# Kernel tuning notes

Measured on AMD Instinct MI355X. Metric: run time of the kernel, lower is better.

Reference implementation:

```python
import jax, jax.numpy as jnp
import numpy as np
import math

HID, H = 384, 4
D = HID // H  # 96, HGT head dim
N_T = [2048, 2048, 2048, 1024, 1024]  # user_turn, ai_turn, stance, pressure, belief
OFF = [0, 2048, 4096, 6144, 7168]
NTOT = 8192
# (src_type, dst_type, num_edges)
EDGES = [(0, 1, 32768), (1, 0, 32768), (1, 2, 32768), (2, 2, 32768),
         (0, 3, 16384), (3, 1, 32768), (1, 4, 16384), (4, 2, 32768)]
E_OFF = np.concatenate([[0], np.cumsum([c for _, _, c in EDGES])]).tolist()


def _gelu(x):
    return jax.nn.gelu(x, approximate=False)


def _ln(x, g, b, eps=1e-5):
    m = x.mean(-1, keepdims=True)
    v = ((x - m) ** 2).mean(-1, keepdims=True)
    return (x - m) * jax.lax.rsqrt(v + eps) * g + b


def _mha(q_in, kv_in, Wqkv, bqkv, Wo, bo):
    # torch nn.MultiheadAttention (batch_first, batch=1); Wqkv stored [E, 3E]
    E = HID
    q = (q_in @ Wqkv[:, :E] + bqkv[:E]).reshape(-1, H, D)
    k = (kv_in @ Wqkv[:, E:2 * E] + bqkv[E:2 * E]).reshape(-1, H, D)
    v = (kv_in @ Wqkv[:, 2 * E:] + bqkv[2 * E:]).reshape(-1, H, D)
    s = jnp.einsum('qhd,khd->hqk', q, k) / math.sqrt(D)
    w = jax.nn.softmax(s, axis=-1)
    o = jnp.einsum('hqk,khd->qhd', w, v).reshape(-1, E)
    return o @ Wo + bo


def _forward(x_user, x_ai, x_stance, x_pressure, x_belief,
             hgt_Wkqv, hgt_bkqv, hgt_Wout, hgt_bout, hgt_krel, hgt_vrel, hgt_prel, hgt_skip,
             ln_g, ln_b, sp_W, sp_b, sp_lng, sp_lnb, fc0_W, fc0_b, bn_g, bn_b,
             tq_W, tq_b, tk_W, tk_b, tv_W, tv_b, mha_Wqkv, mha_bqkv, mha_Wo, mha_bo,
             c1_W, c1_b, c2_W, c2_b, op_W, op_b, as1_W, as1_b, as2_W, as2_b,
             sc1_W, sc1_b, sc2_W, sc2_b, cl1_W, cl1_b, cl_lng, cl_lnb,
             cl2_W, cl2_b, cl3_W, cl3_b, tp_W, tp_b, edge_src, edge_dst):
    xs = [x_user, x_ai, x_stance, x_pressure, x_belief]
    for l in range(2):
        kqv = [x @ hgt_Wkqv[l, t] + hgt_bkqv[l, t] for t, x in enumerate(xs)]
        kk = [a[:, :HID].reshape(-1, H, D) for a in kqv]
        qq = [a[:, HID:2 * HID].reshape(-1, H, D) for a in kqv]
        vv = [a[:, 2 * HID:].reshape(-1, H, D) for a in kqv]
        al, msg, dgl = [], [], []
        for r, (s, d, cnt) in enumerate(EDGES):
            si = edge_src[E_OFF[r]:E_OFF[r + 1]]
            di = edge_dst[E_OFF[r]:E_OFF[r + 1]]
            ke = jnp.einsum('ehd,hdf->ehf', kk[s][si], hgt_krel[l, r])
            ve = jnp.einsum('ehd,hdf->ehf', vv[s][si], hgt_vrel[l, r])
            a = (qq[d][di] * ke).sum(-1) * hgt_prel[l, r] / math.sqrt(D)  # [E_r, H]
            al.append(a); msg.append(ve); dgl.append(di + OFF[d])
        a = jnp.concatenate(al); ve = jnp.concatenate(msg); dg = jnp.concatenate(dgl)
        mx = jax.ops.segment_max(a, dg, num_segments=NTOT)
        ex = jnp.exp(a - mx[dg])
        den = jax.ops.segment_sum(ex, dg, num_segments=NTOT)
        w = ex / den[dg]
        agg = jax.ops.segment_sum(ve * w[:, :, None], dg, num_segments=NTOT).reshape(NTOT, HID)
        new = []
        for t, x in enumerate(xs):
            o = _gelu(agg[OFF[t]:OFF[t] + N_T[t]]) @ hgt_Wout[l, t] + hgt_bout[l, t]
            g = jax.nn.sigmoid(hgt_skip[l, t])
            new.append(g * o + (1 - g) * x)
        xs = [_ln(_gelu(v), ln_g[t], ln_b[t]) for t, v in enumerate(new)]
    user_h, ai_h, stance_h, pressure_h, belief_h = xs

    # ---- StanceTrajectoryEncoder ----
    hs = _gelu(_ln(stance_h @ sp_W + sp_b, sp_lng, sp_lnb))

    def bn(x, i):  # eval-mode BatchNorm1d, running stats (0, 1)
        return x * (bn_g[i] / math.sqrt(1.0 + 1e-5)) + bn_b[i]

    xg = jax.nn.relu(bn(hs @ fc0_W + fc0_b, 0))
    Ns = hs.shape[0]
    for i in range(2):  # SGFormer TransConv layers (linear global attention)
        q = (xg @ tq_W[i] + tq_b[i]).reshape(Ns, H, HID)
        k = (xg @ tk_W[i] + tk_b[i]).reshape(Ns, H, HID)
        v = (xg @ tv_W[i] + tv_b[i]).reshape(Ns, H, HID)
        qn = q / jnp.linalg.norm(q)  # global Frobenius norm, as in SGFormer
        kn = k / jnp.linalg.norm(k)
        kvs = jnp.einsum('lhm,lhd->hmd', kn, v)
        num = jnp.einsum('nhm,hmd->nhd', qn, kvs) + Ns * v
        dnm = jnp.einsum('nhm,hm->nh', qn, kn.sum(0))[:, :, None] + Ns
        z = (num / dnm).mean(axis=1)  # mean over heads
        xg = jax.nn.relu(bn(0.5 * z + 0.5 * xg, i + 1))  # residual alpha=0.5
    h_mixed = 0.7 * hs + 0.3 * xg
    traj = _mha(h_mixed, h_mixed, mha_Wqkv[1], mha_bqkv[1], mha_Wo[1], mha_bo[1])
    traj_summary = traj.mean(0, keepdims=True)  # [1, HID]
    ci = h_mixed.T[None]  # [1, C, L]
    dn = ('NCH', 'OIH', 'NCH')
    c = jax.lax.conv_general_dilated(ci, c1_W, (1,), [(1, 1)], dimension_numbers=dn) + c1_b[None, :, None]
    c = _gelu(c)
    c = jax.lax.conv_general_dilated(c, c2_W, (1,), [(1, 1)], dimension_numbers=dn) + c2_b[None, :, None]
    c = _gelu(c)
    decay_summary = c.mean(axis=2)  # [1, HID//2]
    traj_emb = jnp.concatenate([traj_summary, decay_summary], -1) @ op_W + op_b

    # ---- PressureResponseModule ----
    ai_ctx = _mha(ai_h, user_h, mha_Wqkv[0], mha_bqkv[0], mha_Wo[0], mha_bo[0])
    ml = min(N_T[1], N_T[0])
    comb = jnp.concatenate([ai_h[:ml], user_h[:ml]], -1)
    pscores = jax.nn.sigmoid((jax.nn.relu(comb @ as1_W + as1_b) @ as2_W + as2_b)[:, 0])
    ai_pooled = ai_ctx.mean(0, keepdims=True)

    # ---- belief attention + stance comparison + classifier ----
    bctx = _mha(ai_h, belief_h, mha_Wqkv[2], mha_bqkv[2], mha_Wo[2], mha_bo[2]).mean(0, keepdims=True)
    sd_in = jnp.concatenate([stance_h[0:1], stance_h[-1:]], -1)
    stance_delta = jax.nn.relu(sd_in @ sc1_W + sc1_b) @ sc2_W + sc2_b
    comb2 = jnp.concatenate([traj_emb, ai_pooled, bctx, stance_delta], -1)  # [1, 1344]
    z = jax.nn.relu(_ln(comb2 @ cl1_W + cl1_b, cl_lng, cl_lnb))
    z = jax.nn.relu(z @ cl2_W + cl2_b)
    logits = (z @ cl3_W + cl3_b).reshape(())
    decay = jax.nn.sigmoid(logits)
    per_turn = jax.nn.sigmoid((ai_ctx @ tp_W + tp_b)[:, 0])
    return logits, decay, per_turn, pscores


def setup_inputs() -> dict:
    key = jax.random.key(0)
    ks = iter(jax.random.split(key, 128))

    def P(shape, fan_in):
        return jax.random.normal(next(ks), shape, jnp.float32) / np.float32(math.sqrt(fan_in))

    inp = {}
    for name, n in zip(['x_user', 'x_ai', 'x_stance', 'x_pressure', 'x_belief'], N_T):
        inp[name] = jax.random.normal(next(ks), (n, HID), jnp.float32)
    inp['hgt_Wkqv'] = P((2, 5, HID, 3 * HID), HID)
    inp['hgt_bkqv'] = jnp.zeros((2, 5, 3 * HID))
    inp['hgt_Wout'] = P((2, 5, HID, HID), HID)
    inp['hgt_bout'] = jnp.zeros((2, 5, HID))
    inp['hgt_krel'] = P((2, 8, H, D, D), D)
    inp['hgt_vrel'] = P((2, 8, H, D, D), D)
    inp['hgt_prel'] = jnp.ones((2, 8, H))
    inp['hgt_skip'] = jnp.ones((2, 5))
    inp['ln_g'] = jnp.ones((5, HID)); inp['ln_b'] = jnp.zeros((5, HID))
    inp['sp_W'] = P((HID, HID), HID); inp['sp_b'] = jnp.zeros((HID,))
    inp['sp_lng'] = jnp.ones((HID,)); inp['sp_lnb'] = jnp.zeros((HID,))
    inp['fc0_W'] = P((HID, HID), HID); inp['fc0_b'] = jnp.zeros((HID,))
    inp['bn_g'] = jnp.ones((3, HID)); inp['bn_b'] = jnp.zeros((3, HID))
    for nm in ['tq', 'tk', 'tv']:
        inp[nm + '_W'] = P((2, HID, H * HID), HID)
        inp[nm + '_b'] = jnp.zeros((2, H * HID))
    inp['mha_Wqkv'] = P((3, HID, 3 * HID), HID)
    inp['mha_bqkv'] = jnp.zeros((3, 3 * HID))
    inp['mha_Wo'] = P((3, HID, HID), HID)
    inp['mha_bo'] = jnp.zeros((3, HID))
    inp['c1_W'] = P((HID, HID, 3), HID * 3); inp['c1_b'] = jnp.zeros((HID,))
    inp['c2_W'] = P((HID // 2, HID, 3), HID * 3); inp['c2_b'] = jnp.zeros((HID // 2,))
    inp['op_W'] = P((HID + HID // 2, HID), HID + HID // 2); inp['op_b'] = jnp.zeros((HID,))
    inp['as1_W'] = P((2 * HID, HID), 2 * HID); inp['as1_b'] = jnp.zeros((HID,))
    inp['as2_W'] = P((HID, 1), HID); inp['as2_b'] = jnp.zeros((1,))
    inp['sc1_W'] = P((2 * HID, HID), 2 * HID); inp['sc1_b'] = jnp.zeros((HID,))
    inp['sc2_W'] = P((HID, HID // 2), HID); inp['sc2_b'] = jnp.zeros((HID // 2,))
    CIN = 3 * HID + HID // 2
    inp['cl1_W'] = P((CIN, HID), CIN); inp['cl1_b'] = jnp.zeros((HID,))
    inp['cl_lng'] = jnp.ones((HID,)); inp['cl_lnb'] = jnp.zeros((HID,))
    inp['cl2_W'] = P((HID, HID // 2), HID); inp['cl2_b'] = jnp.zeros((HID // 2,))
    inp['cl3_W'] = P((HID // 2, 1), HID // 2); inp['cl3_b'] = jnp.zeros((1,))
    inp['tp_W'] = P((HID, 1), HID); inp['tp_b'] = jnp.zeros((1,))
    srcs, dsts = [], []
    for (s, d, cnt) in EDGES:
        srcs.append(jax.random.randint(next(ks), (cnt,), 0, N_T[s], jnp.int32))
        dsts.append(jax.random.randint(next(ks), (cnt,), 0, N_T[d], jnp.int32))
    inp['edge_src'] = jnp.concatenate(srcs)
    inp['edge_dst'] = jnp.concatenate(dsts)
    return inp


def reference(x_user, x_ai, x_stance, x_pressure, x_belief,
              hgt_Wkqv, hgt_bkqv, hgt_Wout, hgt_bout, hgt_krel, hgt_vrel, hgt_prel, hgt_skip,
              ln_g, ln_b, sp_W, sp_b, sp_lng, sp_lnb, fc0_W, fc0_b, bn_g, bn_b,
              tq_W, tq_b, tk_W, tk_b, tv_W, tv_b, mha_Wqkv, mha_bqkv, mha_Wo, mha_bo,
              c1_W, c1_b, c2_W, c2_b, op_W, op_b, as1_W, as1_b, as2_W, as2_b,
              sc1_W, sc1_b, sc2_W, sc2_b, cl1_W, cl1_b, cl_lng, cl_lnb,
              cl2_W, cl2_b, cl3_W, cl3_b, tp_W, tp_b, edge_src, edge_dst):
    return _forward(x_user, x_ai, x_stance, x_pressure, x_belief,
                    hgt_Wkqv, hgt_bkqv, hgt_Wout, hgt_bout, hgt_krel, hgt_vrel, hgt_prel, hgt_skip,
                    ln_g, ln_b, sp_W, sp_b, sp_lng, sp_lnb, fc0_W, fc0_b, bn_g, bn_b,
                    tq_W, tq_b, tk_W, tk_b, tv_W, tv_b, mha_Wqkv, mha_bqkv, mha_Wo, mha_bo,
                    c1_W, c1_b, c2_W, c2_b, op_W, op_b, as1_W, as1_b, as2_W, as2_b,
                    sc1_W, sc1_b, sc2_W, sc2_b, cl1_W, cl1_b, cl_lng, cl_lnb,
                    cl2_W, cl2_b, cl3_W, cl3_b, tp_W, tp_b, edge_src, edge_dst)
```

## Files before the change

kernel.cpp:

```cpp
#include <hip/hip_runtime.h>
#include <hip/hip_bf16.h>

#define NEDGE 229376
#define NTOT  8192
#define BNCONST 0.9999950000374997f
#define ISQ96   0.10206207261596575f

__constant__ int c_NT[5]     = {2048,2048,2048,1024,1024};
__constant__ int c_OFFS[5]   = {0,2048,4096,6144,7168};
__constant__ int c_ESRC[8]   = {0,1,1,2,0,3,1,4};
__constant__ int c_EDST[8]   = {1,0,2,2,3,1,4,2};
__constant__ int c_EOFF[9]   = {0,32768,65536,98304,131072,147456,180224,196608,229376};
__constant__ int c_RELROW[8] = {0,2048,4096,6144,8192,10240,11264,13312};

static const int h_NT[5]   = {2048,2048,2048,1024,1024};
static const int h_OFFS[5] = {0,2048,4096,6144,7168};

__device__ inline float gelu_f(float x){ return 0.5f*x*(1.0f+erff(x*0.70710678118654752f)); }
__device__ inline float sigm(float x){ return 1.0f/(1.0f+expf(-x)); }
__device__ inline float wsum64(float v){
  #pragma unroll
  for (int s=32;s>0;s>>=1) v += __shfl_xor(v, s, 64);
  return v;
}
// ... 18 lines not shown
__device__ inline float rgsum(float v){
  v += __shfl_xor(v, 1, 64);
  v += __shfl_xor(v, 2, 64);
  v += __shfl_xor(v, 4, 64);
  v += __shfl_xor(v, 8, 64);
  return v;
}


__global__ void k_mix(const float* __restrict__ a, const float* __restrict__ b,
                      float* __restrict__ c, int n, float fa, float fb){
  int i = blockIdx.x*256 + threadIdx.x;
  if (i < n) c[i] = fa*a[i] + fb*b[i];
}

__global__ void k_comb(const float* __restrict__ ai, const float* __restrict__ user,
                       float* __restrict__ cb){
  int i = blockIdx.x*256 + threadIdx.x;
  if (i >= 2048*768) return;
  int n = i / 768, c = i - n*768;
  cb[i] = (c < 384) ? ai[n*384 + c] : user[n*384 + (c-384)];
}


__global__ void k_edge_pre(const int* __restrict__ esrc, const int* __restrict__ edst,
                           int* edg, int* esr, int* erl, int* cnt){
  int e = blockIdx.x*256 + threadIdx.x;
  if (e >= NEDGE) return;
  int r = 0;
  #pragma unroll
  for (int q=1;q<8;q++) if (e >= c_EOFF[q]) r = q;
  int dg = c_OFFS[c_EDST[r]] + edst[e];
  edg[e] = dg;
  esr[e] = c_RELROW[r] + esrc[e];
  erl[e] = r;
  atomicAdd(&cnt[dg], 1);
}

__global__ __launch_bounds__(1024) void k_scan(const int* __restrict__ cnt, int* __restrict__ off){
  __shared__ int sh[1024];
  int tid = threadIdx.x;
  int base = tid*8;
  int loc[8]; int run = 0;
  #pragma unroll
  for (int i=0;i<8;i++){ loc[i] = run; run += cnt[base+i]; }
  sh[tid] = run;
  __syncthreads();
  for (int d=1; d<1024; d<<=1){
    int v = (tid >= d) ? sh[tid-d] : 0;
    __syncthreads();
    sh[tid] += v;
    __syncthreads();
  }
  int pre = (tid==0) ? 0 : sh[tid-1];
  #pragma unroll
  for (int i=0;i<8;i++) off[base+i] = pre + loc[i];
  if (tid==1023) off[8192] = sh[1023];
}

__global__ void k_scatter(const int* __restrict__ edg, const int* __restrict__ off,
                          int* cnt2, int* csr){
  int e = blockIdx.x*256 + threadIdx.x;
  if (e >= NEDGE) return;
  int dg = edg[e];
  int pos = off[dg] + atomicAdd(&cnt2[dg], 1);
  csr[pos] = e;
}


__global__ __launch_bounds__(256) void gemm_f(
    const float* __restrict__ A, int lda, const float* __restrict__ B, int ldb,
    const float* __restrict__ bias, const float* __restrict__ cs, const float* __restrict__ csh,
    float kmul, float* __restrict__ C, int ldc, int M, int N, int K, int act, int agelu)
{
  __shared__ float As[2][16][68];
  __shared__ float Bs[2][16][68];
  int tid = threadIdx.x;
  int tx = tid & 15, ty = tid >> 4;
  int am = tid >> 2, ak = (tid & 3) * 4;
  int bk = tid >> 4, bn = (tid & 15) * 4;
  int m0 = blockIdx.y * 64, n0 = blockIdx.x * 64;
  int gmA = m0 + am;
  int gnB = n0 + bn;
  int ntiles = K >> 4;
  float4 ra, rb;
  float acc[4][4] = {};

  auto fetch = [&](int kk){
    if (gmA < M){
      ra = *reinterpret_cast<const float4*>(&A[(size_t)gmA*lda + kk + ak]);
      if (agelu){ ra.x=gelu_f(ra.x); ra.y=gelu_f(ra.y); ra.z=gelu_f(ra.z); ra.w=gelu_f(ra.w); }
    } else ra = make_float4(0.f,0.f,0.f,0.f);
    if (gnB + 3 < N){
      rb = *reinterpret_cast<const float4*>(&B[(size_t)(kk + bk)*ldb + gnB]);
    } else {
      rb.x = (gnB   < N) ? B[(size_t)(kk + bk)*ldb + gnB  ] : 0.f;
      rb.y = (gnB+1 < N) ? B[(size_t)(kk + bk)*ldb + gnB+1] : 0.f;
      rb.z = (gnB+2 < N) ? B[(size_t)(kk + bk)*ldb + gnB+2] : 0.f;
      rb.w = (gnB+3 < N) ? B[(size_t)(kk + bk)*ldb + gnB+3] : 0.f;
    }
  };
  auto stage = [&](int b){
    As[b][ak  ][am] = ra.x;
    As[b][ak+1][am] = ra.y;
    As[b][ak+2][am] = ra.z;
    As[b][ak+3][am] = ra.w;
    *reinterpret_cast<float4*>(&Bs[b][bk][bn]) = rb;
  };

  fetch(0);
  stage(0);
  __syncthreads();
  for (int t = 0; t < ntiles; t++){
    int cur = t & 1;
    if (t + 1 < ntiles) fetch((t+1) << 4);
    #pragma unroll
    for (int k = 0; k < 16; k++) {
      float4 a4 = *reinterpret_cast<const float4*>(&As[cur][k][ty*4]);
      float4 b4 = *reinterpret_cast<const float4*>(&Bs[cur][k][tx*4]);
      float a[4] = {a4.x, a4.y, a4.z, a4.w};
      float b[4] = {b4.x, b4.y, b4.z, b4.w};
      #pragma unroll
      for (int i=0;i<4;i++)
        #pragma unroll
        for (int j=0;j<4;j++) acc[i][j] += a[i]*b[j];
    }
    if (t + 1 < ntiles) stage(cur ^ 1);
    __syncthreads();
  }
  #pragma unroll
  for (int i=0;i<4;i++){
    int gm = m0 + ty*4 + i; if (gm >= M) continue;
    #pragma unroll
    for (int j=0;j<4;j++){
      int gn = n0 + tx*4 + j; if (gn >= N) continue;
      float v = acc[i][j];
      if (bias) v += bias[gn];
      float s = kmul;
      if (cs) s *= cs[gn];
      v *= s;
      if (csh) v += csh[gn];
      if (act==1) v = fmaxf(v, 0.f);
      else if (act==2) v = gelu_f(v);
      C[(size_t)gm*ldc + gn] = v;
    }
  }
}

__global__ __launch_bounds__(256) void gemm128(
    const float* __restrict__ A, int lda, int sAz,
    const float* __restrict__ B, int ldb, int sBz,
    const float* __restrict__ bias, int sbz,
    float* __restrict__ C, int ldc, int sCz,
    int M, int N, int K, int act, int agelu, int tsel)
{
  __shared__ float As[2][16][132];
  __shared__ float Bs[2][16][132];
  int tid = threadIdx.x;
  int tx = tid & 15, ty = tid >> 4;
  int am = tid >> 1, ak = (tid & 1) * 8;
  int bk = tid >> 4, bn = (tid & 15) * 8;
  int m0 = blockIdx.y * 128, n0 = blockIdx.x * 128;
  int z = blockIdx.z;
  const float* Ab = A + (size_t)z * sAz;
  const float* Bb = B + (size_t)z * sBz;
  const float* bb = bias ? (bias + (size_t)z * sbz) : nullptr;
  float* Cb = C + (size_t)z * sCz;
  if (tsel){
    int t = row_type(m0);
    Bb = B + (size_t)t * sBz;
    bb = bias ? (bias + (size_t)t * sbz) : nullptr;
  }
  int gmA = m0 + am, gnB = n0 + bn;
  int ntiles = K >> 4;
  float4 ra0, ra1, rb0, rb1;
  float acc[8][8] = {};

  auto fetch = [&](int kk){
    if (gmA < M){
      ra0 = *reinterpret_cast<const float4*>(&Ab[(size_t)gmA*lda + kk + ak]);
      ra1 = *reinterpret_cast<const float4*>(&Ab[(size_t)gmA*lda + kk + ak + 4]);
      if (agelu){
        ra0.x=gelu_f(ra0.x); ra0.y=gelu_f(ra0.y); ra0.z=gelu_f(ra0.z); ra0.w=gelu_f(ra0.w);
        ra1.x=gelu_f(ra1.x); ra1.y=gelu_f(ra1.y); ra1.z=gelu_f(ra1.z); ra1.w=gelu_f(ra1.w);
      }
    } else {
      ra0 = make_float4(0.f,0.f,0.f,0.f); ra1 = ra0;
    }
    if (gnB + 7 < N){
      rb0 = *reinterpret_cast<const float4*>(&Bb[(size_t)(kk + bk)*ldb + gnB]);
      rb1 = *reinterpret_cast<const float4*>(&Bb[(size_t)(kk + bk)*ldb + gnB + 4]);
    } else {
      const float* bp = &Bb[(size_t)(kk + bk)*ldb];
      rb0.x = (gnB   < N) ? bp[gnB  ] : 0.f;
      rb0.y = (gnB+1 < N) ? bp[gnB+1] : 0.f;
      rb0.z = (gnB+2 < N) ? bp[gnB+2] : 0.f;
      rb0.w = (gnB+3 < N) ? bp[gnB+3] : 0.f;
      rb1.x = (gnB+4 < N) ? bp[gnB+4] : 0.f;
      rb1.y = (gnB+5 < N) ? bp[gnB+5] : 0.f;
      rb1.z = (gnB+6 < N) ? bp[gnB+6] : 0.f;
      rb1.w = (gnB+7 < N) ? bp[gnB+7] : 0.f;
    }
  };
  auto stage = [&](int b){
    As[b][ak  ][am] = ra0.x;
    As[b][ak+1][am] = ra0.y;
    As[b][ak+2][am] = ra0.z;
    As[b][ak+3][am] = ra0.w;
    As[b][ak+4][am] = ra1.x;
    As[b][ak+5][am] = ra1.y;
    As[b][ak+6][am] = ra1.z;
    As[b][ak+7][am] = ra1.w;
    *reinterpret_cast<float4*>(&Bs[b][bk][bn  ]) = rb0;
    *reinterpret_cast<float4*>(&Bs[b][bk][bn+4]) = rb1;
  };

  fetch(0);
  stage(0);
  __syncthreads();
  for (int t = 0; t < ntiles; t++){
    int cur = t & 1;
    if (t + 1 < ntiles) fetch((t+1) << 4);
    #pragma unroll
    for (int k = 0; k < 16; k++) {
      float4 a0 = *reinterpret_cast<const float4*>(&As[cur][k][ty*8]);
      float4 a1 = *reinterpret_cast<const float4*>(&As[cur][k][ty*8+4]);
      float4 b0 = *reinterpret_cast<const float4*>(&Bs[cur][k][tx*8]);
      float4 b1 = *reinterpret_cast<const float4*>(&Bs[cur][k][tx*8+4]);
      float a[8] = {a0.x,a0.y,a0.z,a0.w,a1.x,a1.y,a1.z,a1.w};
      float b[8] = {b0.x,b0.y,b0.z,b0.w,b1.x,b1.y,b1.z,b1.w};
      #pragma unroll
      for (int i=0;i<8;i++)
        #pragma unroll
        for (int j=0;j<8;j++) acc[i][j] += a[i]*b[j];
    }
    if (t + 1 < ntiles) stage(cur ^ 1);
    __syncthreads();
  }

  bool fullN = (n0 + 127 < N);
  #pragma unroll
  for (int i=0;i<8;i++){
    int gm = m0 + ty*8 + i; if (gm >= M) continue;
    float v[8];
    #pragma unroll
    for (int j=0;j<8;j++){
      float x = acc[i][j];
      if (bb){
        int gn = n0 + tx*8 + j;
        if (gn < N) x += bb[gn];
      }
      if (act==1) x = fmaxf(x, 0.f);
      else if (act==2) x = gelu_f(x);
      v[j] = x;
    }
    if (fullN){
      *reinterpret_cast<float4*>(&Cb[(size_t)gm*ldc + n0 + tx*8    ]) = make_float4(v[0],v[1],v[2],v[3]);
      *reinterpret_cast<float4*>(&Cb[(size_t)gm*ldc + n0 + tx*8 + 4]) = make_float4(v[4],v[5],v[6],v[7]);
    } else {
      #pragma unroll
      for (int j=0;j<8;j++){
        int gn = n0 + tx*8 + j; if (gn >= N) continue;
        Cb[(size_t)gm*ldc + gn] = v[j];
      }
    }
  }
}

__global__ __launch_bounds__(256) void gemm_rel(
    const float* __restrict__ KQV_, const float* __restrict__ krel_l,
    const float* __restrict__ vrel_l, float* __restrict__ KE_, float* __restrict__ VE_)
{
  int z = blockIdx.z;
  int w = z & 1, h = (z >> 1) & 3, r = z >> 3;
  int s = c_ESRC[r];
  int Ns = c_NT[s];
  int m0 = blockIdx.y * 64;
  if (m0 >= Ns) return;
  int n0 = blockIdx.x * 64;
  const float* A = KQV_ + (size_t)c_OFFS[s]*1152 + (w ? 768 : 0) + h*96;
  const float* B = (w ? vrel_l : krel_l) + (size_t)(r*4 + h)*9216;
  float* C = (w ? VE_ : KE_) + (size_t)c_RELROW[r]*384 + h*96;

  __shared__ float As[2][16][68];
  __shared__ float Bs[2][16][68];
  int tid = threadIdx.x;
  int tx = tid & 15, ty = tid >> 4;
  int am = tid >> 2, ak = (tid & 3) * 4;
  int bk = tid >> 4, bn = (tid & 15) * 4;
  int gmA = m0 + am;
  int gnB = n0 + bn;
  float4 ra, rb;
  float acc[4][4] = {};

  auto fetch = [&](int kk){
    ra = (gmA < Ns) ? *reinterpret_cast<const float4*>(&A[(size_t)gmA*1152 + kk + ak])
                    : make_float4(0.f,0.f,0.f,0.f);
    if (gnB + 3 < 96){
      rb = *reinterpret_cast<const float4*>(&B[(size_t)(kk + bk)*96 + gnB]);
    } else {
      rb.x = (gnB   < 96) ? B[(size_t)(kk + bk)*96 + gnB  ] : 0.f;
      rb.y = (gnB+1 < 96) ? B[(size_t)(kk + bk)*96 + gnB+1] : 0.f;
      rb.z = (gnB+2 < 96) ? B[(size_t)(kk + bk)*96 + gnB+2] : 0.f;
      rb.w = (gnB+3 < 96) ? B[(size_t)(kk + bk)*96 + gnB+3] : 0.f;
    }
  };
  auto stage = [&](int b){
    As[b][ak  ][am] = ra.x;
    As[b][ak+1][am] = ra.y;
    As[b][ak+2][am] = ra.z;
    As[b][ak+3][am] = ra.w;
    *reinterpret_cast<float4*>(&Bs[b][bk][bn]) = rb;
  };

  fetch(0);
  stage(0);
  __syncthreads();
  for (int t = 0; t < 6; t++){
    int cur = t & 1;
    if (t + 1 < 6) fetch((t+1) << 4);
    #pragma unroll
    for (int k = 0; k < 16; k++) {
      float4 a4 = *reinterpret_cast<const float4*>(&As[cur][k][ty*4]);
      float4 b4 = *reinterpret_cast<const float4*>(&Bs[cur][k][tx*4]);
      float a[4] = {a4.x, a4.y, a4.z, a4.w};
      float b[4] = {b4.x, b4.y, b4.z, b4.w};
      #pragma unroll
      for (int i=0;i<4;i++)
        #pragma unroll
        for (int j=0;j<4;j++) acc[i][j] += a[i]*b[j];
    }
    if (t + 1 < 6) stage(cur ^ 1);
    __syncthreads();
  }
  #pragma unroll
  for (int i=0;i<4;i++){
    int gm = m0 + ty*4 + i; if (gm >= Ns) continue;
    #pragma unroll
    for (int j=0;j<4;j++){
      int gn = n0 + tx*4 + j; if (gn >= 96) continue;
      C[(size_t)gm*384 + gn] = acc[i][j];
    }
  }
}

__global__ __launch_bounds__(256) void gemm_atb_ks(
    const float* __restrict__ A0, int lda, const float* __restrict__ B0, int ldb,
    float* __restrict__ C0, int ldc, int M, int N, int L,
    int hsA, int hsB, int hsC, int nch)
{
  __shared__ float As[2][16][68];
  __shared__ float Bs[2][16][68];
  int h = blockIdx.z / nch, c = blockIdx.z % nch;
  const float* A = A0 + (size_t)h*hsA;
  const float* B = B0 + (size_t)h*hsB;
  float* C = C0 + (size_t)h*hsC;
  int l0 = c*256;
  int tid = threadIdx.x;
  int tx = tid & 15, ty = tid >> 4;
  int sl = tid >> 4, sq = (tid & 15) * 4;
  int m0 = blockIdx.y * 64, n0 = blockIdx.x * 64;
  int gmA = m0 + sq, gnB = n0 + sq;
  int ntiles = 16;
  float4 ra, rb;
  float acc[4][4] = {};

  auto fetch = [&](int ll){
    if (gmA + 3 < M){
      ra = *reinterpret_cast<const float4*>(&A[(size_t)(ll + sl)*lda + gmA]);
    } else {
      ra.x = (gmA   < M) ? A[(size_t)(ll + sl)*lda + gmA  ] : 0.f;
      ra.y = (gmA+1 < M) ? A[(size_t)(ll + sl)*lda + gmA+1] : 0.f;
      ra.z = (gmA+2 < M) ? A[(size_t)(ll + sl)*lda + gmA+2] : 0.f;
      ra.w = (gmA+3 < M) ? A[(size_t)(ll + sl)*lda + gmA+3] : 0.f;
    }
    if (gnB + 3 < N){
      rb = *reinterpret_cast<const float4*>(&B[(size_t)(ll + sl)*ldb + gnB]);
    } else {
      rb.x = (gnB   < N) ? B[(size_t)(ll + sl)*ldb + gnB  ] : 0.f;
      rb.y = (gnB+1 < N) ? B[(size_t)(ll + sl)*ldb + gnB+1] : 0.f;
      rb.z = (gnB+2 < N) ? B[(size_t)(ll + sl)*ldb + gnB+2] : 0.f;
      rb.w = (gnB+3 < N) ? B[(size_t)(ll + sl)*ldb + gnB+3] : 0.f;
    }
  };
  auto stage = [&](int b){
    *reinterpret_cast<float4*>(&As[b][sl][sq]) = ra;
    *reinterpret_cast<float4*>(&Bs[b][sl][sq]) = rb;
  };

  fetch(l0);
  stage(0);
  __syncthreads();
  for (int t = 0; t < ntiles; t++){
    int cur = t & 1;
    if (t + 1 < ntiles) fetch(l0 + ((t+1) << 4));
    #pragma unroll
    for (int l = 0; l < 16; l++) {
      float4 a4 = *reinterpret_cast<const float4*>(&As[cur][l][ty*4]);
      float4 b4 = *reinterpret_cast<const float4*>(&Bs[cur][l][tx*4]);
      float a[4] = {a4.x, a4.y, a4.z, a4.w};
      float b[4] = {b4.x, b4.y, b4.z, b4.w};
      #pragma unroll
      for (int i=0;i<4;i++)
        #pragma unroll
        for (int j=0;j<4;j++) acc[i][j] += a[i]*b[j];
    }
    if (t + 1 < ntiles) stage(cur ^ 1);
    __syncthreads();
  }
  #pragma unroll
  for (int i=0;i<4;i++){
    int gm = m0 + ty*4 + i; if (gm >= M) continue;
    #pragma unroll
    for (int j=0;j<4;j++){
      int gn = n0 + tx*4 + j; if (gn >= N) continue;
      atomicAdd(&C[(size_t)gm*ldc + gn], acc[i][j]);
// ... 373 lines not shown
    const float* __restrict__ w, const float* __restrict__ b, float* __restrict__ out, int M){
  int r = blockIdx.x*4 + (threadIdx.x>>6);
  if (r >= M) return;
  int lane = threadIdx.x & 63;
  const float* a = A + (size_t)r*lda;
  float p = 0.f;
  for (int k = lane; k < K; k += 64) p += a[k]*w[k];
  p = wsum64(p);
  if (lane==0) out[r] = sigm(p + b[0]);
}

__global__ __launch_bounds__(64) void k_final(const float* __restrict__ z2,
    const float* __restrict__ w, const float* __restrict__ b, float* __restrict__ out){
  int lane = threadIdx.x;
  float p = 0.f;
  for (int k = lane; k < 192; k += 64) p += z2[k]*w[k];
  p = wsum64(p);
  if (lane==0){
    float l = p + b[0];
    out[0] = l;
    out[1] = sigm(l);
  }
}


extern "C" void kernel_launch(void* const* d_in, const int* in_sizes, int n_in,
                              void* d_out, int out_size, void* d_ws, size_t ws_size,
                              hipStream_t stream)
{
  const float* xin[5] = {(const float*)d_in[0], (const float*)d_in[1], (const float*)d_in[2],
                         (const float*)d_in[3], (const float*)d_in[4]};
  const float* Wkqv=(const float*)d_in[5];  const float* bkqv=(const float*)d_in[6];
  const float* Wout=(const float*)d_in[7];  const float* bout=(const float*)d_in[8];
  const float* krel=(const float*)d_in[9];  const float* vrel=(const float*)d_in[10];
  const float* prel=(const float*)d_in[11]; const float* skp =(const float*)d_in[12];
  const float* lng =(const float*)d_in[13]; const float* lnb =(const float*)d_in[14];
  const float* sp_W=(const float*)d_in[15]; const float* sp_b=(const float*)d_in[16];
  const float* sp_lng=(const float*)d_in[17]; const float* sp_lnb=(const float*)d_in[18];
  const float* fc0_W=(const float*)d_in[19]; const float* fc0_b=(const float*)d_in[20];
  const float* bn_g=(const float*)d_in[21]; const float* bn_b=(const float*)d_in[22];
  const float* tq_W=(const float*)d_in[23]; const float* tq_b=(const float*)d_in[24];
  const float* tk_W=(const float*)d_in[25]; const float* tk_b=(const float*)d_in[26];
  const float* tv_W=(const float*)d_in[27]; const float* tv_b=(const float*)d_in[28];
  const float* mWqkv=(const float*)d_in[29]; const float* mbqkv=(const float*)d_in[30];
  const float* mWo=(const float*)d_in[31];  const float* mbo=(const float*)d_in[32];
  const float* c1W=(const float*)d_in[33];  const float* c1b=(const float*)d_in[34];
  const float* c2W=(const float*)d_in[35];  const float* c2b=(const float*)d_in[36];
  const float* opW=(const float*)d_in[37];  const float* opb=(const float*)d_in[38];
  const float* as1W=(const float*)d_in[39]; const float* as1b=(const float*)d_in[40];
  const float* as2W=(const float*)d_in[41]; const float* as2b=(const float*)d_in[42];
  const float* sc1W=(const float*)d_in[43]; const float* sc1b=(const float*)d_in[44];
  const float* sc2W=(const float*)d_in[45]; const float* sc2b=(const float*)d_in[46];
  const float* cl1W=(const float*)d_in[47]; const float* cl1b=(const float*)d_in[48];
  const float* cllng=(const float*)d_in[49]; const float* cllnb=(const float*)d_in[50];
  const float* cl2W=(const float*)d_in[51]; const float* cl2b=(const float*)d_in[52];
  const float* cl3W=(const float*)d_in[53]; const float* cl3b=(const float*)d_in[54];
  const float* tpW=(const float*)d_in[55];  const float* tpb=(const float*)d_in[56];
  const int* e_src=(const int*)d_in[57];  const int* e_dst=(const int*)d_in[58];
  float* out = (float*)d_out;

  char* ws = (char*)d_ws;
  size_t off_b = 0;
  auto alloc = [&](size_t bytes)->char*{
    char* r = ws + off_b;
    off_b = (off_b + bytes + 255) & ~(size_t)255;
    return r;
  };
  float* X    = (float*)alloc((size_t)8192*384*4);
  float* KQV  = (float*)alloc((size_t)8192*1152*4);
  float* KE   = (float*)alloc((size_t)14336*384*4);
  float* VE   = (float*)alloc((size_t)14336*384*4);
  float* AGG  = (float*)alloc((size_t)8192*384*4);
  float* EA   = (float*)alloc((size_t)NEDGE*4*4);
  int* edg    = (int*)alloc((size_t)NEDGE*4);
  int* esr    = (int*)alloc((size_t)NEDGE*4);
  int* erl    = (int*)alloc((size_t)NEDGE*4);
  int* csr    = (int*)alloc((size_t)NEDGE*4);
  int* cnt    = (int*)alloc(8192*4);
  int* cnt2   = (int*)alloc(8192*4);
  int* coff   = (int*)alloc(8193*4);
  unsigned* EMX = (unsigned*)alloc(8192*4*4);
  float* EDEN = (float*)alloc(8192*4*4);
  float* SM   = (float*)alloc(65536);
  float* GT   = (float*)alloc(20*384*4);
  if (off_b > ws_size) return;

  float* SQSK = SM;
  float* TRAJSUM = SM + 8;
  float* DECAYSUM = SM + 392;
  float* TEMB = SM + 600;
  float* AIPOOL = SM + 984;
  float* BCTXV = SM + 1368;
  float* SDELT = SM + 1752;
  float* SDIN = SM + 2048;
  float* T1   = SM + 2816;
  float* Z1   = SM + 3200;
  float* Zb   = SM + 3584;
  float* Z2   = SM + 3968;
  float* KSUM = SM + 4224;
  float* DNM  = SM + 6144;

  float* QB = KQV;
  float* KB = KQV + (size_t)2048*1536;
  float* VB = KQV + (size_t)2*2048*1536;
  float* MQKV = KQV;
  float* AO = KQV + (size_t)2*2048*1536;
  float* ZNUM = KE;
  float* OWT = KE;
  float* OPART = KE;
  float* MLBUF = KE + (size_t)3200000;
  float* IMC = KE;
  float* WT  = KE + (size_t)2400000;
  float* HS = VE;
  float* XG = VE + (size_t)2048*384;
  float* HM = VE + (size_t)2*2048*384;
  float* C1O = VE + (size_t)3*2048*384;
  float* TRAJ = VE + (size_t)4*2048*384;
  float* AICTX = VE + (size_t)5*2048*384;
  float* C2O = VE + (size_t)6*2048*384;
  float* TMPA = AGG;
  float* CB = AGG;
  float* PT = AGG + (size_t)2048*768;
  float* KVS = AGG + (size_t)2048*1152;

  dim3 B256(256);
  auto gemm = [&](const float* A, int lda, const float* Bw, int ldb, const float* bias,
                  const float* cs, const float* csh, float kmul,
                  float* C, int ldc, int M, int N, int K, int act, int agelu){
    dim3 g((N+63)/64, (M+63)/64);
    gemm_f<<<g, B256, 0, stream>>>(A, lda, Bw, ldb, bias, cs, csh, kmul, C, ldc, M, N, K, act, agelu);
  };
  auto gemv = [&](const float* in, int K, const float* W, int ldw, const float* b,
                  float* o, int N, int act){
    int nk = (K + 79) / 80; if (nk > 20) nk = 20; if (nk < 1) nk = 1;
    k_gemv_ks<<<dim3((N+63)/64, nk), B256, 0, stream>>>(in, K, W, ldw, GT, N);
    k_gemv_fin<<<dim3((N+255)/256), B256, 0, stream>>>(GT, nk, b, o, N, act);
  };

  hipMemsetAsync(cnt, 0, 8192*4, stream);
  hipMemsetAsync(cnt2, 0, 8192*4, stream);
  k_edge_pre<<<dim3(NEDGE/256), B256, 0, stream>>>(e_src, e_dst, edg, esr, erl, cnt);
  k_scan<<<dim3(1), dim3(1024), 0, stream>>>(cnt, coff);
  k_scatter<<<dim3(NEDGE/256), B256, 0, stream>>>(edg, coff, cnt2, csr);

  for (int t=0;t<5;t++)
    hipMemcpyAsync(X + (size_t)h_OFFS[t]*384, xin[t], (size_t)h_NT[t]*384*4,
                   hipMemcpyDeviceToDevice, stream);

  for (int l=0;l<2;l++){
    gemm128<<<dim3(9, 64), B256, 0, stream>>>(
        X, 384, 0,
        Wkqv + (size_t)l*5*442368, 1152, 442368,
        bkqv + (size_t)l*5*1152, 1152,
        KQV, 1152, 0, 8192, 1152, 384, 0, 0, 1 );
    gemm_rel<<<dim3(2,32,64), B256, 0, stream>>>(
        KQV, krel + (size_t)l*294912, vrel + (size_t)l*294912, KE, VE);
    k_escore<<<dim3(NEDGE/4), B256, 0, stream>>>(KQV, KE, edg, esr, erl, prel + (size_t)l*32, EA);
    hipMemsetAsync(EMX, 0, 8192*4*4, stream);
    hipMemsetAsync(EDEN, 0, 8192*4*4, stream);
    k_segmax<<<dim3(NEDGE*4/256), B256, 0, stream>>>(EA, edg, EMX);
    k_expsum<<<dim3(NEDGE*4/256), B256, 0, stream>>>(EA, edg, EMX, EDEN);
    k_agg<<<dim3(NTOT), dim3(128), 0, stream>>>(EA, VE, EDEN, csr, coff, esr, AGG);
    gemm128<<<dim3(3, 64), B256, 0, stream>>>(
        AGG, 384, 0,
        Wout + (size_t)l*5*147456, 384, 147456,
        bout + (size_t)l*5*384, 384,
        OWT, 384, 0, 8192, 384, 384, 0, 1 , 1 );
    k_gateln<<<dim3(NTOT), dim3(128), 0, stream>>>(OWT, X, skp + l*5, lng, lnb);
  }

  const float* user_h   = X;
  const float* ai_h     = X + (size_t)2048*384;
  const float* stance_h = X + (size_t)4096*384;
  const float* belief_h = X + (size_t)7168*384;

  gemm(stance_h, 384, sp_W, 384, sp_b, nullptr, nullptr, 1.f, TMPA, 384, 2048, 384, 384, 0, 0);
  k_lnrow<<<dim3(2048), dim3(128), 0, stream>>>(TMPA, HS, sp_lng, sp_lnb, 0 );
  gemm(HS, 384, fc0_W, 384, fc0_b, bn_g, bn_b, BNCONST, XG, 384, 2048, 384, 384, 1 , 0);

  for (int i=0;i<2;i++){
    gemm128<<<dim3(12,16), B256, 0, stream>>>(
        XG, 384, 0, tq_W + (size_t)i*589824, 1536, 0,
        tq_b + (size_t)i*1536, 0, QB, 1536, 0, 2048, 1536, 384, 0, 0, 0);
    gemm128<<<dim3(12,16), B256, 0, stream>>>(
        XG, 384, 0, tk_W + (size_t)i*589824, 1536, 0,
        tk_b + (size_t)i*1536, 0, KB, 1536, 0, 2048, 1536, 384, 0, 0, 0);
    gemm128<<<dim3(12,16), B256, 0, stream>>>(
        XG, 384, 0, tv_W + (size_t)i*589824, 1536, 0,
        tv_b + (size_t)i*1536, 0, VB, 1536, 0, 2048, 1536, 384, 0, 0, 0);
    hipMemsetAsync(SQSK, 0, 8, stream);
    k_sumsq<<<dim3(512), B256, 0, stream>>>(QB, 2048*1536, SQSK);
    k_sumsq<<<dim3(512), B256, 0, stream>>>(KB, 2048*1536, SQSK+1);
    hipMemsetAsync(KSUM, 0, 1536*4, stream);
    k_colsum<<<dim3(6,8), B256, 0, stream>>>(KB, 2048, 1536, 1.0f, KSUM);
    k_dnm<<<dim3(2048), B256, 0, stream>>>(QB, KSUM, SQSK, DNM);
    hipMemsetAsync(KVS, 0, (size_t)4*147456*4, stream);
    gemm_atb_ks<<<dim3(6,6,32), B256, 0, stream>>>(KB, 1536, VB, 1536, KVS, 384,
        384, 384, 2048, 384, 384, 147456, 8);
    gemm128<<<dim3(3,16,4), B256, 0, stream>>>(
        QB, 1536, 384, KVS, 384, 147456,
        nullptr, 0, ZNUM, 1536, 384, 2048, 384, 384, 0, 0, 0);
    k_zcomb<<<dim3(3072), B256, 0, stream>>>(ZNUM, VB, DNM, SQSK, XG,
        bn_g + (size_t)(i+1)*384, bn_b + (size_t)(i+1)*384);
  }

  k_mix<<<dim3(3072), B256, 0, stream>>>(HS, XG, HM, 2048*384, 0.7f, 0.3f);

  auto run_mha = [&](const float* qin, int nq, const float* kvin, int nkv, int mi, float* OUT){
    const float* Wq = mWqkv + (size_t)mi*442368;
    const float* bq = mbqkv + (size_t)mi*1152;
    gemm(qin, 384, Wq, 1152, bq, nullptr, nullptr, 1.f, MQKV, 1152, nq, 384, 384, 0, 0);
    gemm(kvin, 384, Wq + 384, 1152, bq + 384, nullptr, nullptr, 1.f, MQKV + 384, 1152, nkv, 768, 384, 0, 0);
    int nch = nkv / 512;
    fa_kernel<<<dim3(nq/64, 4, nch), B256, 0, stream>>>(MQKV, nq, OPART, MLBUF);
    k_famerge<<<dim3((4*nq*96 + 255)/256), B256, 0, stream>>>(OPART, MLBUF, AO, nq, nch);
    gemm(AO, 384, mWo + (size_t)mi*147456, 384, mbo + (size_t)mi*384,
         nullptr, nullptr, 1.f, OUT, 384, nq, 384, 384, 0, 0);
  };

  run_mha(HM, 2048, HM, 2048, 1, TRAJ);
  hipMemsetAsync(TRAJSUM, 0, 576*4, stream);
  k_colsum<<<dim3(2,8), B256, 0, stream>>>(TRAJ, 2048, 384, 1.0f/2048.0f, TRAJSUM);

  k_im2col<<<dim3(2048*1152/256), B256, 0, stream>>>(HM, IMC);
  k_wtr<<<dim3((384*1152+255)/256), B256, 0, stream>>>(c1W, WT, 384);
  gemm(IMC, 1152, WT, 384, c1b, nullptr, nullptr, 1.f, C1O, 384, 2048, 384, 1152, 2 , 0);
  k_im2col<<<dim3(2048*1152/256), B256, 0, stream>>>(C1O, IMC);
  k_wtr<<<dim3((192*1152+255)/256), B256, 0, stream>>>(c2W, WT, 192);
  gemm(IMC, 1152, WT, 192, c2b, nullptr, nullptr, 1.f, C2O, 192, 2048, 192, 1152, 2 , 0);
  k_colsum<<<dim3(1,8), B256, 0, stream>>>(C2O, 2048, 192, 1.0f/2048.0f, DECAYSUM);

  gemv(TRAJSUM, 576, opW, 384, opb, TEMB, 384, 0);

  run_mha(ai_h, 2048, user_h, 2048, 0, AICTX);
  hipMemsetAsync(AIPOOL, 0, 384*4, stream);
  k_colsum<<<dim3(2,8), B256, 0, stream>>>(AICTX, 2048, 384, 1.0f/2048.0f, AIPOOL);

  k_comb<<<dim3(6144), B256, 0, stream>>>(ai_h, user_h, CB);
  gemm(CB, 768, as1W, 384, as1b, nullptr, nullptr, 1.f, PT, 384, 2048, 384, 768, 1, 0);
  k_rowdot<<<dim3(512), B256, 0, stream>>>(PT, 384, 384, as2W, as2b, out + 2 + 2048, 2048);

  run_mha(ai_h, 2048, belief_h, 1024, 2, TRAJ);
  hipMemsetAsync(BCTXV, 0, 384*4, stream);
  k_colsum<<<dim3(2,8), B256, 0, stream>>>(TRAJ, 2048, 384, 1.0f/2048.0f, BCTXV);

  hipMemcpyAsync(SDIN, stance_h, 384*4, hipMemcpyDeviceToDevice, stream);
  hipMemcpyAsync(SDIN + 384, stance_h + (size_t)2047*384, 384*4, hipMemcpyDeviceToDevice, stream);
  gemv(SDIN, 768, sc1W, 384, sc1b, T1, 384, 1);
  gemv(T1, 384, sc2W, 192, sc2b, SDELT, 192, 0);

  gemv(TEMB, 1344, cl1W, 384, cl1b, Z1, 384, 0);
  k_lnrow<<<dim3(1), dim3(128), 0, stream>>>(Z1, Zb, cllng, cllnb, 1 );
  gemv(Zb, 384, cl2W, 192, cl2b, Z2, 192, 1);
  k_final<<<dim3(1), dim3(64), 0, stream>>>(Z2, cl3W, cl3b, out);

  k_rowdot<<<dim3(512), B256, 0, stream>>>(AICTX, 384, 384, tpW, tpb, out + 2, 2048);
}
```

Before: 3.510 ms.

## Restructure gemm128 thread mapping, remap blocks across XCDs, batch Q/K/V projections

Each thread in gemm128 now owns two 4-wide strided column and row groups instead of one contiguous 8-wide group. This changes the LDS read and global store patterns and should cut LDS bank conflicts. Workgroup IDs are remapped so that neighbouring output tiles land on the same XCD, which is meant to improve L2 reuse. The three separate Q/K/V projection launches become a single z=3 launch with per-z weight and bias pointers. That launch assumes QB, KB and VB are laid out contiguously with stride 2048*1536, and it breaks if they are not.

```diff
diff --git a/kernel.cpp b/kernel.cpp
--- a/kernel.cpp
+++ b/kernel.cpp
@@ -194,19 +194,36 @@
     const float* __restrict__ B, int ldb, int sBz,
     const float* __restrict__ bias, int sbz,
     float* __restrict__ C, int ldc, int sCz,
-    int M, int N, int K, int act, int agelu, int tsel)
+    int M, int N, int K, int act, int agelu, int tsel,
+    const float* __restrict__ Bp1, const float* __restrict__ Bp2,
+    const float* __restrict__ biasp1, const float* __restrict__ biasp2)
 {
   __shared__ float As[2][16][132];
   __shared__ float Bs[2][16][132];
   int tid = threadIdx.x;
   int tx = tid & 15, ty = tid >> 4;
   int am = tid >> 1, ak = (tid & 1) * 8;
-  int bk = tid >> 4, bn = (tid & 15) * 8;
-  int m0 = blockIdx.y * 128, n0 = blockIdx.x * 128;
+  int bk = tid >> 4, bn = (tid & 15) * 4;
+
+  int nxy = gridDim.x * gridDim.y;
+  int orig = blockIdx.y * gridDim.x + blockIdx.x;
+  int q = nxy >> 3, r = nxy & 7;
+  int xcd = orig & 7, rest = orig >> 3;
+  int wg = ((xcd < r) ? xcd*(q+1) : r*(q+1) + (xcd - r)*q) + rest;
+  int bx = wg % gridDim.x, by = wg / gridDim.x;
+  int m0 = by * 128, n0 = bx * 128;
+
   int z = blockIdx.z;
   const float* Ab = A + (size_t)z * sAz;
-  const float* Bb = B + (size_t)z * sBz;
-  const float* bb = bias ? (bias + (size_t)z * sbz) : nullptr;
+  const float* Bb;
+  const float* bb;
+  if (Bp1){
+    Bb = (z == 0) ? B : ((z == 1) ? Bp1 : Bp2);
+    bb = (z == 0) ? bias : ((z == 1) ? biasp1 : biasp2);
+  } else {
+    Bb = B + (size_t)z * sBz;
+    bb = bias ? (bias + (size_t)z * sbz) : nullptr;
+  }
   float* Cb = C + (size_t)z * sCz;
   if (tsel){
     int t = row_type(m0);
@@ -229,19 +246,19 @@
     } else {
       ra0 = make_float4(0.f,0.f,0.f,0.f); ra1 = ra0;
     }
-    if (gnB + 7 < N){
+    if (gnB + 67 < N){
       rb0 = *reinterpret_cast<const float4*>(&Bb[(size_t)(kk + bk)*ldb + gnB]);
-      rb1 = *reinterpret_cast<const float4*>(&Bb[(size_t)(kk + bk)*ldb + gnB + 4]);
+      rb1 = *reinterpret_cast<const float4*>(&Bb[(size_t)(kk + bk)*ldb + gnB + 64]);
     } else {
       const float* bp = &Bb[(size_t)(kk + bk)*ldb];
-      rb0.x = (gnB   < N) ? bp[gnB  ] : 0.f;
-      rb0.y = (gnB+1 < N) ? bp[gnB+1] : 0.f;
-      rb0.z = (gnB+2 < N) ? bp[gnB+2] : 0.f;
-      rb0.w = (gnB+3 < N) ? bp[gnB+3] : 0.f;
-      rb1.x = (gnB+4 < N) ? bp[gnB+4] : 0.f;
-      rb1.y = (gnB+5 < N) ? bp[gnB+5] : 0.f;
-      rb1.z = (gnB+6 < N) ? bp[gnB+6] : 0.f;
-      rb1.w = (gnB+7 < N) ? bp[gnB+7] : 0.f;
+      rb0.x = (gnB    < N) ? bp[gnB   ] : 0.f;
+      rb0.y = (gnB+1  < N) ? bp[gnB+ 1] : 0.f;
+      rb0.z = (gnB+2  < N) ? bp[gnB+ 2] : 0.f;
+      rb0.w = (gnB+3  < N) ? bp[gnB+ 3] : 0.f;
+      rb1.x = (gnB+64 < N) ? bp[gnB+64] : 0.f;
+      rb1.y = (gnB+65 < N) ? bp[gnB+65] : 0.f;
+      rb1.z = (gnB+66 < N) ? bp[gnB+66] : 0.f;
+      rb1.w = (gnB+67 < N) ? bp[gnB+67] : 0.f;
     }
   };
   auto stage = [&](int b){
@@ -253,8 +270,8 @@
     As[b][ak+5][am] = ra1.y;
     As[b][ak+6][am] = ra1.z;
     As[b][ak+7][am] = ra1.w;
-    *reinterpret_cast<float4*>(&Bs[b][bk][bn  ]) = rb0;
-    *reinterpret_cast<float4*>(&Bs[b][bk][bn+4]) = rb1;
+    *reinterpret_cast<float4*>(&Bs[b][bk][bn     ]) = rb0;
+    *reinterpret_cast<float4*>(&Bs[b][bk][bn + 64]) = rb1;
   };
 
   fetch(0);
@@ -265,10 +282,10 @@
     if (t + 1 < ntiles) fetch((t+1) << 4);
     #pragma unroll
     for (int k = 0; k < 16; k++) {
-      float4 a0 = *reinterpret_cast<const float4*>(&As[cur][k][ty*8]);
-      float4 a1 = *reinterpret_cast<const float4*>(&As[cur][k][ty*8+4]);
-      float4 b0 = *reinterpret_cast<const float4*>(&Bs[cur][k][tx*8]);
-      float4 b1 = *reinterpret_cast<const float4*>(&Bs[cur][k][tx*8+4]);
+      float4 a0 = *reinterpret_cast<const float4*>(&As[cur][k][ty*4]);
+      float4 a1 = *reinterpret_cast<const float4*>(&As[cur][k][64 + ty*4]);
+      float4 b0 = *reinterpret_cast<const float4*>(&Bs[cur][k][tx*4]);
+      float4 b1 = *reinterpret_cast<const float4*>(&Bs[cur][k][64 + tx*4]);
       float a[8] = {a0.x,a0.y,a0.z,a0.w,a1.x,a1.y,a1.z,a1.w};
       float b[8] = {b0.x,b0.y,b0.z,b0.w,b1.x,b1.y,b1.z,b1.w};
       #pragma unroll
@@ -281,29 +298,38 @@
   }
 
   bool fullN = (n0 + 127 < N);
-  #pragma unroll
-  for (int i=0;i<8;i++){
-    int gm = m0 + ty*8 + i; if (gm >= M) continue;
-    float v[8];
+  int cb0 = n0 + tx*4, cb1 = n0 + 64 + tx*4;
+  #pragma unroll
+  for (int ih=0; ih<2; ih++){
     #pragma unroll
-    for (int j=0;j<8;j++){
-      float x = acc[i][j];
-      if (bb){
-        int gn = n0 + tx*8 + j;
-        if (gn < N) x += bb[gn];
+    for (int i=0;i<4;i++){
+      int gm = m0 + ih*64 + ty*4 + i;
+      if (gm >= M) continue;
+      float v[8];
+      #pragma unroll
+      for (int jh=0; jh<2; jh++){
+        #pragma unroll
+        for (int j=0;j<4;j++){
+          float x = acc[ih*4+i][jh*4+j];
+          int gn = (jh ? cb1 : cb0) + j;
+          if (bb && gn < N) x += bb[gn];
+          if (act==1) x = fmaxf(x, 0.f);
+          else if (act==2) x = gelu_f(x);
+          v[jh*4+j] = x;
+        }
       }
-      if (act==1) x = fmaxf(x, 0.f);
-      else if (act==2) x = gelu_f(x);
-      v[j] = x;
-    }
-    if (fullN){
-      *reinterpret_cast<float4*>(&Cb[(size_t)gm*ldc + n0 + tx*8    ]) = make_float4(v[0],v[1],v[2],v[3]);
-      *reinterpret_cast<float4*>(&Cb[(size_t)gm*ldc + n0 + tx*8 + 4]) = make_float4(v[4],v[5],v[6],v[7]);
-    } else {
-      #pragma unroll
-      for (int j=0;j<8;j++){
-        int gn = n0 + tx*8 + j; if (gn >= N) continue;
-        Cb[(size_t)gm*ldc + gn] = v[j];
+      if (fullN){
+        *reinterpret_cast<float4*>(&Cb[(size_t)gm*ldc + cb0]) = make_float4(v[0],v[1],v[2],v[3]);
+        *reinterpret_cast<float4*>(&Cb[(size_t)gm*ldc + cb1]) = make_float4(v[4],v[5],v[6],v[7]);
+      } else {
+        #pragma unroll
+        for (int jh=0; jh<2; jh++){
+          #pragma unroll
+          for (int j=0;j<4;j++){
+            int gn = (jh ? cb1 : cb0) + j;
+            if (gn < N) Cb[(size_t)gm*ldc + gn] = v[jh*4+j];
+          }
+        }
       }
     }
   }
@@ -983,7 +1009,8 @@
         X, 384, 0,
         Wkqv + (size_t)l*5*442368, 1152, 442368,
         bkqv + (size_t)l*5*1152, 1152,
-        KQV, 1152, 0, 8192, 1152, 384, 0, 0, 1 );
+        KQV, 1152, 0, 8192, 1152, 384, 0, 0, 1 ,
+        nullptr, nullptr, nullptr, nullptr);
     gemm_rel<<<dim3(2,32,64), B256, 0, stream>>>(
         KQV, krel + (size_t)l*294912, vrel + (size_t)l*294912, KE, VE);
     k_escore<<<dim3(NEDGE/4), B256, 0, stream>>>(KQV, KE, edg, esr, erl, prel + (size_t)l*32, EA);
@@ -996,7 +1023,8 @@
         AGG, 384, 0,
         Wout + (size_t)l*5*147456, 384, 147456,
         bout + (size_t)l*5*384, 384,
-        OWT, 384, 0, 8192, 384, 384, 0, 1 , 1 );
+        OWT, 384, 0, 8192, 384, 384, 0, 1 , 1 ,
+        nullptr, nullptr, nullptr, nullptr);
     k_gateln<<<dim3(NTOT), dim3(128), 0, stream>>>(OWT, X, skp + l*5, lng, lnb);
   }
 
@@ -1010,15 +1038,14 @@
   gemm(HS, 384, fc0_W, 384, fc0_b, bn_g, bn_b, BNCONST, XG, 384, 2048, 384, 384, 1 , 0);
 
   for (int i=0;i<2;i++){
-    gemm128<<<dim3(12,16), B256, 0, stream>>>(
-        XG, 384, 0, tq_W + (size_t)i*589824, 1536, 0,
-        tq_b + (size_t)i*1536, 0, QB, 1536, 0, 2048, 1536, 384, 0, 0, 0);
-    gemm128<<<dim3(12,16), B256, 0, stream>>>(
-        XG, 384, 0, tk_W + (size_t)i*589824, 1536, 0,
-        tk_b + (size_t)i*1536, 0, KB, 1536, 0, 2048, 1536, 384, 0, 0, 0);
-    gemm128<<<dim3(12,16), B256, 0, stream>>>(
-        XG, 384, 0, tv_W + (size_t)i*589824, 1536, 0,
-        tv_b + (size_t)i*1536, 0, VB, 1536, 0, 2048, 1536, 384, 0, 0, 0);
+    gemm128<<<dim3(12,16,3), B256, 0, stream>>>(
+        XG, 384, 0,
+        tq_W + (size_t)i*589824, 1536, 0,
+        tq_b + (size_t)i*1536, 0,
+        QB, 1536, 2048*1536,
+        2048, 1536, 384, 0, 0, 0,
+        tk_W + (size_t)i*589824, tv_W + (size_t)i*589824,
+        tk_b + (size_t)i*1536, tv_b + (size_t)i*1536);
     hipMemsetAsync(SQSK, 0, 8, stream);
     k_sumsq<<<dim3(512), B256, 0, stream>>>(QB, 2048*1536, SQSK);
     k_sumsq<<<dim3(512), B256, 0, stream>>>(KB, 2048*1536, SQSK+1);
@@ -1030,7 +1057,8 @@
         384, 384, 2048, 384, 384, 147456, 8);
     gemm128<<<dim3(3,16,4), B256, 0, stream>>>(
         QB, 1536, 384, KVS, 384, 147456,
-        nullptr, 0, ZNUM, 1536, 384, 2048, 384, 384, 0, 0, 0);
+        nullptr, 0, ZNUM, 1536, 384, 2048, 384, 384, 0, 0, 0,
+        nullptr, nullptr, nullptr, nullptr);
     k_zcomb<<<dim3(3072), B256, 0, stream>>>(ZNUM, VB, DNM, SQSK, XG,
         bn_g + (size_t)(i+1)*384, bn_b + (size_t)(i+1)*384);
   }
```

Measured after the change: 3.388 ms. -3.5%, faster.
